# Kernel tuning notes

Hardware: AMD Instinct MI355X
Metric: run time of the kernel (lower is better)

The kernel has to match this reference:

```python
import jax, jax.numpy as jnp
import numpy as np

D_STATE = 16
D_CONV = 4
DT_RANK = 2  # ceil(d_model/16) with d_model=32


def _conv2d(x, w, b, pad, dil=1, groups=1):
    y = jax.lax.conv_general_dilated(
        x, w, (1, 1), ((pad, pad), (pad, pad)), rhs_dilation=(dil, dil),
        feature_group_count=groups, dimension_numbers=('NCHW', 'OIHW', 'NCHW'))
    return y + b[None, :, None, None]


def _ssm(xc, delta, A, Bc, Cc, D):
    # xc,delta: (B,L,Di); A: (Di,N); Bc,Cc: (B,L,N)
    dA = jnp.exp(delta[..., None] * A)                       # (B,L,Di,N)
    dBx = delta[..., None] * Bc[:, :, None, :] * xc[..., None]
    def comb(e1, e2):
        a1, b1 = e1
        a2, b2 = e2
        return a2 * a1, a2 * b1 + b2
    _, h = jax.lax.associative_scan(comb, (dA, dBx), axis=1)  # h_t = dA_t*h_{t-1}+dBx_t
    return jnp.einsum('bldn,bln->bld', h, Cc) + xc * D


def _dir(xin, cw, cb, wx, wdt, bdt, A_log, D):
    # causal depthwise conv1d over L, then silu
    L = xin.shape[1]
    xp = jnp.pad(xin, ((0, 0), (D_CONV - 1, 0), (0, 0)))
    xc = sum(xp[:, k:k + L, :] * cw[:, k] for k in range(D_CONV)) + cb
    xc = jax.nn.silu(xc)
    dbc = xc @ wx.T                                          # (B,L,dt_rank+2N)
    dt, Bc, Cc = jnp.split(dbc, [DT_RANK, DT_RANK + D_STATE], axis=-1)
    delta = jax.nn.softplus(dt @ wdt.T + bdt)
    return _ssm(xc, delta, -jnp.exp(A_log), Bc, Cc, D)


def _mamba(xn, w_in, cwf, cbf, wxf, wdtf, bdtf, Af, Df,
           cwb, cbb, wxb, wdtb, bdtb, Ab, Db, w_out):
    xz = xn @ w_in.T                                         # (B,L,2*Di)
    xin, z = jnp.split(xz, 2, axis=-1)
    y_f = _dir(xin, cwf, cbf, wxf, wdtf, bdtf, Af, Df)
    y_b = jnp.flip(_dir(jnp.flip(xin, axis=1), cwb, cbb, wxb, wdtb, bdtb, Ab, Db), axis=1)
    return ((y_f + y_b) * jax.nn.silu(z)) @ w_out.T          # bimamba v2: sum of directions


def _forward(x, w_att, b_att, ln_w, ln_b, w_in,
             conv_w_f, conv_b_f, wx_f, wdt_f, bdt_f, A_log_f, D_f,
             conv_w_b, conv_b_b, wx_b, wdt_b, bdt_b, A_log_b, D_b,
             w_out, w_se, b_se, w_conv, b_conv):
    B, C, H, W = x.shape
    att1 = x
    xa = _conv2d(x, w_att, b_att, pad=9, dil=3, groups=C)    # dilated depthwise, same HxW
    xf = xa.reshape(B, C, H * W).transpose(0, 2, 1)          # (B,L,C)
    mu = xf.mean(-1, keepdims=True)
    var = xf.var(-1, keepdims=True)
    xn = (xf - mu) / jnp.sqrt(var + 1e-5) * ln_w + ln_b
    out = _mamba(xn, w_in, conv_w_f, conv_b_f, wx_f, wdt_f, bdt_f, A_log_f, D_f,
                 conv_w_b, conv_b_b, wx_b, wdt_b, bdt_b, A_log_b, D_b, w_out)
    att2 = out.transpose(0, 2, 1).reshape(B, C, H, W)
    att = jnp.concatenate([att1, att2], axis=1)
    pooled = jnp.concatenate([att.mean(1, keepdims=True), att.max(1, keepdims=True)], axis=1)
    se = jax.nn.sigmoid(_conv2d(pooled, w_se, b_se, pad=3))
    output = att1 * se[:, 0:1] + att2 * se[:, 1:2]
    return _conv2d(output, w_conv, b_conv, pad=1)


def setup_inputs() -> dict:
    key = jax.random.key(0)
    ks = jax.random.split(key, 16)
    B, C, H, W = 4, 32, 96, 96
    Di, OUT = 64, 64
    n = jax.random.normal
    A_log = jnp.tile(jnp.log(jnp.arange(1, D_STATE + 1, dtype=jnp.float32)), (Di, 1))
    return {
        'x': n(ks[0], (B, C, H, W), jnp.float32),
        'w_att': n(ks[1], (C, 1, 7, 7), jnp.float32) * 0.05,
        'b_att': jnp.zeros((C,), jnp.float32),
        'ln_w': jnp.ones((C,), jnp.float32),
        'ln_b': jnp.zeros((C,), jnp.float32),
        'w_in': n(ks[2], (2 * Di, C), jnp.float32) / np.sqrt(C),
        'conv_w_f': n(ks[3], (Di, D_CONV), jnp.float32) * 0.3,
        'conv_b_f': jnp.zeros((Di,), jnp.float32),
        'wx_f': n(ks[4], (DT_RANK + 2 * D_STATE, Di), jnp.float32) / np.sqrt(Di),
        'wdt_f': n(ks[5], (Di, DT_RANK), jnp.float32) * 0.5,
        'bdt_f': n(ks[6], (Di,), jnp.float32) * 0.1,
        'A_log_f': A_log,
        'D_f': jnp.ones((Di,), jnp.float32),
        'conv_w_b': n(ks[7], (Di, D_CONV), jnp.float32) * 0.3,
        'conv_b_b': jnp.zeros((Di,), jnp.float32),
        'wx_b': n(ks[8], (DT_RANK + 2 * D_STATE, Di), jnp.float32) / np.sqrt(Di),
        'wdt_b': n(ks[9], (Di, DT_RANK), jnp.float32) * 0.5,
        'bdt_b': n(ks[10], (Di,), jnp.float32) * 0.1,
        'A_log_b': A_log,
        'D_b': jnp.ones((Di,), jnp.float32),
        'w_out': n(ks[11], (C, Di), jnp.float32) / np.sqrt(Di),
        'w_se': n(ks[12], (2, 2, 7, 7), jnp.float32) * 0.1,
        'b_se': jnp.zeros((2,), jnp.float32),
        'w_conv': n(ks[13], (OUT, C, 3, 3), jnp.float32) * 0.06,
        'b_conv': jnp.zeros((OUT,), jnp.float32),
    }


def reference(x, w_att, b_att, ln_w, ln_b, w_in,
              conv_w_f, conv_b_f, wx_f, wdt_f, bdt_f, A_log_f, D_f,
              conv_w_b, conv_b_b, wx_b, wdt_b, bdt_b, A_log_b, D_b,
              w_out, w_se, b_se, w_conv, b_conv):
    return _forward(x, w_att, b_att, ln_w, ln_b, w_in,
                    conv_w_f, conv_b_f, wx_f, wdt_f, bdt_f, A_log_f, D_f,
                    conv_w_b, conv_b_b, wx_b, wdt_b, bdt_b, A_log_b, D_b,
                    w_out, w_se, b_se, w_conv, b_conv)
```

## Files before the change

### kernel.cpp

```cpp
#include <hip/hip_runtime.h>
#include <math.h>

#define BB 4
#define CH 32
#define HH 96
#define WW 96
#define LL (HH*WW)
#define DI 64
#define NS 16
#define BL (BB*LL)
#define NCH 288
#define CLEN (LL/NCH)
#define GG 8

__device__ __forceinline__ float sigmoidf_(float x){ return 1.f/(1.f+__expf(-x)); }
__device__ __forceinline__ float siluf_(float x){ return x*sigmoidf_(x); }
__device__ __forceinline__ float softplusf_(float x){
  return (x > 15.f) ? x : __logf(1.f + __expf(x));
}
#define WAVE_LDS_FENCE() do { asm volatile("s_waitcnt lgkmcnt(0)" ::: "memory"); __builtin_amdgcn_sched_barrier(0); } while(0)

__global__ __launch_bounds__(256) void k1_conv_att(
    const float* __restrict__ x, const float* __restrict__ w,
    const float* __restrict__ bias, float* __restrict__ xa){
  int idx = blockIdx.x*256 + threadIdx.x;
  if (idx >= BB*CH*LL) return;
  int w0 = idx % WW; int h0 = (idx/WW) % HH; int c = (idx/LL) % CH;
  const float* xp = x + (idx/LL)*LL;
  const float* wp = w + c*49;
  float acc = bias[c];
  #pragma unroll
  for (int kh=0; kh<7; ++kh){
    int hh = h0 + 3*kh - 9;
    if ((unsigned)hh >= HH) continue;
    const float* row = xp + hh*WW;
    #pragma unroll
    for (int kw=0; kw<7; ++kw){
      int ww = w0 + 3*kw - 9;
      if ((unsigned)ww < WW) acc += row[ww]*wp[kh*7+kw];
    }
  }
  xa[idx] = acc;
}

__global__ __launch_bounds__(128) void k2_ln_inproj(
    const float* __restrict__ xa, const float* __restrict__ w_in,
    const float* __restrict__ ln_w, const float* __restrict__ ln_b,
    float* __restrict__ xin, float* __restrict__ zs){
  __shared__ float xs[CH*36];
  __shared__ float smu[32], srs[32];
  int tid = threadIdx.x;
  int tg0 = blockIdx.x*32;
  int bb = tg0 / LL;
  int l0 = tg0 % LL;
  const float* xab = xa + bb*CH*LL + l0;
  for (int r=0; r<8; ++r){
    int idx = r*128 + tid;
    int c = idx >> 5, t = idx & 31;
    xs[c*36+t] = xab[c*LL + t];
  }
  int j = tid;
  float wlj[CH];
  float swl=0.f, bj=0.f;
  #pragma unroll
  for (int c=0;c<CH;++c){
    float wv = ln_w[c]*w_in[j*CH+c];
    wlj[c] = wv; swl += wv;
    bj += ln_b[c]*w_in[j*CH+c];
  }
  __syncthreads();
  if (tid < 32){
    float s=0.f, s2=0.f;
    #pragma unroll
    for (int c=0;c<CH;++c){ float v = xs[c*36+tid]; s+=v; s2+=v*v; }
    float mu = s*(1.f/CH);
    float var = s2*(1.f/CH) - mu*mu;
    smu[tid]=mu; srs[tid]=rsqrtf(var+1e-5f);
  }
  __syncthreads();
  for (int t4=0;t4<8;++t4){
    float a0=0.f,a1=0.f,a2=0.f,a3=0.f;
    #pragma unroll
    for (int c=0;c<CH;++c){
      float4 xv = *(const float4*)&xs[c*36 + t4*4];
      float wv = wlj[c];
      a0 += xv.x*wv; a1 += xv.y*wv; a2 += xv.z*wv; a3 += xv.w*wv;
    }
    float av[4] = {a0,a1,a2,a3};
    #pragma unroll
    for (int q=0;q<4;++q){
      int t = t4*4+q;
      float out = srs[t]*(av[q] - smu[t]*swl) + bj;
      int base = ((bb*LL) + l0 + t)*DI;
      if (j < DI) xin[base + j] = out;
      else        zs[base + (j-DI)] = siluf_(out);
    }
  }
}

__global__ __launch_bounds__(64) void k3_fused(
    const float* __restrict__ xin,
    const float* __restrict__ cw_f, const float* __restrict__ cb_f,
    const float* __restrict__ wx_f, const float* __restrict__ wdt_f, const float* __restrict__ bdt_f,
    const float* __restrict__ Al_f, const float* __restrict__ D_f,
    const float* __restrict__ cw_b, const float* __restrict__ cb_b,
    const float* __restrict__ wx_b, const float* __restrict__ wdt_b, const float* __restrict__ bdt_b,
    const float* __restrict__ Al_b, const float* __restrict__ D_b,
    float* __restrict__ yl_f, float* __restrict__ sp_f, float* __restrict__ Cc_f,
    float* __restrict__ yl_b, float* __restrict__ sp_b, float* __restrict__ Cc_b,
    float* __restrict__ aggP, float* __restrict__ aggS){
  int lane = threadIdx.x;
  int dir = blockIdx.y;
  int bb = blockIdx.z;
  int ch = blockIdx.x;
  int p0 = ch*CLEN;
  const float* cw  = dir? cw_b : cw_f;
  const float* cb  = dir? cb_b : cb_f;
  const float* wx  = dir? wx_b : wx_f;
  const float* wdt = dir? wdt_b : wdt_f;
  const float* bdt = dir? bdt_b : bdt_f;
  const float* Al  = dir? Al_b : Al_f;
  const float* Dv  = dir? D_b : D_f;
  float* ylbuf = dir? yl_b : yl_f;
  float* spbuf = dir? sp_b : sp_f;
  float* Ccb   = dir? Cc_b : Cc_f;

  __shared__ float xcs[GG*64];
  __shared__ float bcs[GG*16];
  __shared__ float ccs[GG*16];
  __shared__ float dtb[GG*2];

  int d = lane;
  float c0=cw[d*4+0], c1=cw[d*4+1], c2=cw[d*4+2], c3=cw[d*4+3], cbv=cb[d];
  float wd0=wdt[d*2], wd1=wdt[d*2+1], bd=bdt[d];
  float Dd = Dv[d];
  float A[NS];
  #pragma unroll
  for (int n4=0;n4<4;++n4){
    float4 av = *(const float4*)&Al[d*NS + n4*4];
    A[n4*4+0] = -__expf(av.x); A[n4*4+1] = -__expf(av.y);
    A[n4*4+2] = -__expf(av.z); A[n4*4+3] = -__expf(av.w);
  }
  float wreg[64];
  if (lane < 34){
    #pragma unroll
    for (int c4=0;c4<16;++c4){
      float4 wv = *(const float4*)&wx[lane*64 + c4*4];
      wreg[c4*4+0]=wv.x; wreg[c4*4+1]=wv.y; wreg[c4*4+2]=wv.z; wreg[c4*4+3]=wv.w;
    }
  }
  float S[NS];
  #pragma unroll
  for (int n=0;n<NS;++n) S[n]=0.f;
  float sdl = 0.f;
  float u1=0.f,u2=0.f,u3=0.f;
  #pragma unroll
  for (int k=1;k<=3;++k){
    int pos = p0 - k;
    float v = 0.f;
    if (pos >= 0){ int ls = dir? (LL-1-pos) : pos; v = xin[(bb*LL+ls)*DI + d]; }
    if(k==1) u1=v; else if(k==2) u2=v; else u3=v;
  }

  const int NG = CLEN/GG;
  float u0buf[GG], u0nxt[GG];
  #pragma unroll
  for (int j=0;j<GG;++j){
    int pos = p0 + j;
    int ls = dir? (LL-1-pos) : pos;
    u0buf[j] = xin[(bb*LL+ls)*DI + d];
  }
  #pragma unroll
  for (int g=0; g<NG; ++g){
    int pbase = p0 + g*GG;
    if (g+1 < NG){
      #pragma unroll
      for (int j=0;j<GG;++j){
        int pos = pbase + GG + j;
        int ls = dir? (LL-1-pos) : pos;
        u0nxt[j] = xin[(bb*LL+ls)*DI + d];
      }
    }
    float xcr[GG];
    #pragma unroll
    for (int j=0;j<GG;++j){
      float u0 = u0buf[j];
      float xc = siluf_(cbv + c0*u3 + c1*u2 + c2*u1 + c3*u0);
      u3=u2; u2=u1; u1=u0;
      xcr[j] = xc;
      xcs[j*64+d] = xc;
    }
    WAVE_LDS_FENCE();
    if (lane < 34){
      #pragma unroll
      for (int j=0;j<GG;++j){
        float acc = 0.f;
        #pragma unroll
        for (int c4=0;c4<16;++c4){
          float4 xv = *(const float4*)&xcs[j*64 + c4*4];
          acc += xv.x*wreg[c4*4+0] + xv.y*wreg[c4*4+1]
               + xv.z*wreg[c4*4+2] + xv.w*wreg[c4*4+3];
        }
        int tb = bb*LL + pbase + j;
        if (lane < 2){
          dtb[j*2+lane] = acc;
        } else if (lane < 18){
          bcs[j*16 + lane-2] = acc;
        } else {
          Ccb[tb*NS + lane-18] = acc;
          ccs[j*16 + lane-18] = acc;
        }
      }
    }
    WAVE_LDS_FENCE();
    #pragma unroll
    for (int j=0;j<GG;++j){
      int tb = bb*LL + pbase + j;
      float dlt = softplusf_(dtb[j*2]*wd0 + dtb[j*2+1]*wd1 + bd);
      sdl += dlt;
      spbuf[tb*DI + d] = sdl;
      float dx = dlt*xcr[j];
      float yv = xcr[j]*Dd;
      #pragma unroll
      for (int n4=0;n4<4;++n4){
        float4 bv = *(const float4*)&bcs[j*16 + n4*4];
        float4 cv = *(const float4*)&ccs[j*16 + n4*4];
        float bvv[4] = {bv.x,bv.y,bv.z,bv.w};
        float cvv[4] = {cv.x,cv.y,cv.z,cv.w};
        #pragma unroll
        for (int q=0;q<4;++q){
          int n = n4*4+q;
          float dA = __expf(dlt*A[n]);
          S[n] = dA*S[n] + dx*bvv[q];
          yv += S[n]*cvv[q];
        }
      }
      ylbuf[tb*DI + d] = yv;
    }
    #pragma unroll
    for (int j=0;j<GG;++j) u0buf[j] = u0nxt[j];
  }
  int bdd = (bb*2+dir)*DI + d;
  float* pp = aggP + (bdd*NCH + ch)*NS;
  float* sp = aggS + (bdd*NCH + ch)*NS;
  #pragma unroll
  for (int n4=0;n4<4;++n4){
    *(float4*)&pp[n4*4] = make_float4(__expf(A[n4*4+0]*sdl),__expf(A[n4*4+1]*sdl),
                                      __expf(A[n4*4+2]*sdl),__expf(A[n4*4+3]*sdl));
    *(float4*)&sp[n4*4] = make_float4(S[n4*4+0],S[n4*4+1],S[n4*4+2],S[n4*4+3]);
  }
}

__global__ __launch_bounds__(256) void p2_scan_agg(
    const float* __restrict__ aggP, const float* __restrict__ aggS,
    float* __restrict__ hin){
  int t = blockIdx.x*256 + threadIdx.x;
  if (t >= BB*2*DI*NS) return;
  int bdd = t >> 4, n = t & 15;
  float h = 0.f;
  #pragma unroll 4
  for (int k=0;k<NCH;++k){
    int i = (bdd*NCH + k)*NS + n;
    float pv = aggP[i], sv = aggS[i];
    hin[i] = h;
    h = pv*h + sv;
  }
}

__global__ __launch_bounds__(256) void k4_outproj(
    const float* __restrict__ yl_f, const float* __restrict__ yl_b,
    const float* __restrict__ sp_f, const float* __restrict__ sp_b,
    const float* __restrict__ Cc_f, const float* __restrict__ Cc_b,
    const float* __restrict__ Al_f, const float* __restrict__ Al_b,
    const float* __restrict__ hin, const float* __restrict__ zs,
    const float* __restrict__ w_out, float* __restrict__ att2){
  __shared__ float ccs_f[32*16], ccs_b[32*16];
  __shared__ float gt[32*64];
  __shared__ float wol[32*65];
  __shared__ float ot[32*33];
  int tid = threadIdx.x;
  int tg0 = blockIdx.x*32;
  int bb = tg0/LL, l0 = tg0%LL;
  int d = tid & 63, tslot = tid >> 6;
  for (int r=0;r<8;++r){
    int idx = r*256+tid;
    wol[(idx>>6)*65 + (idx&63)] = w_out[idx];
  }
  {
    int base_f = (bb*LL + l0)*NS;
    int base_b = (bb*LL + (LL-32-l0))*NS;
    #pragma unroll
    for (int r=0;r<2;++r){
      int idx = r*256+tid;
      ccs_f[idx] = Cc_f[base_f+idx];
      ccs_b[idx] = Cc_b[base_b+idx];
    }
  }
  int ch_f = l0/CLEN;
  int ch_b = (LL-32-l0)/CLEN;
  const float* hpf = hin + (((bb*2+0)*DI + d)*NCH + ch_f)*NS;
  const float* hpb = hin + (((bb*2+1)*DI + d)*NCH + ch_b)*NS;
  float Af[NS], Ab[NS], hf[NS], hb[NS];
  #pragma unroll
  for (int n4=0;n4<4;++n4){
    float4 av = *(const float4*)&Al_f[d*NS + n4*4];
    Af[n4*4+0]=-__expf(av.x); Af[n4*4+1]=-__expf(av.y);
    Af[n4*4+2]=-__expf(av.z); Af[n4*4+3]=-__expf(av.w);
    float4 aw = *(const float4*)&Al_b[d*NS + n4*4];
    Ab[n4*4+0]=-__expf(aw.x); Ab[n4*4+1]=-__expf(aw.y);
    Ab[n4*4+2]=-__expf(aw.z); Ab[n4*4+3]=-__expf(aw.w);
    float4 hv = *(const float4*)&hpf[n4*4];
    hf[n4*4+0]=hv.x; hf[n4*4+1]=hv.y; hf[n4*4+2]=hv.z; hf[n4*4+3]=hv.w;
    float4 hw = *(const float4*)&hpb[n4*4];
    hb[n4*4+0]=hw.x; hb[n4*4+1]=hw.y; hb[n4*4+2]=hw.z; hb[n4*4+3]=hw.w;
  }
  __syncthreads();
  #pragma unroll
  for (int r=0;r<8;++r){
    int tk = tslot*8 + r;
    int l = l0 + tk;
    int tf  = (bb*LL + l)*DI + d;
    int tb2 = (bb*LL + (LL-1-l))*DI + d;
    float spf = sp_f[tf],  yf = yl_f[tf];
    float spb = sp_b[tb2], yb = yl_b[tb2];
    int jb = 31 - tk;
    float fixf = 0.f, fixb = 0.f;
    #pragma unroll
    for (int n=0;n<NS;++n){
      fixf += ccs_f[tk*16+n] * (hf[n]*__expf(Af[n]*spf));
      fixb += ccs_b[jb*16+n] * (hb[n]*__expf(Ab[n]*spb));
    }
    gt[tk*64+d] = (yf+fixf + yb+fixb) * zs[tf];
  }
  __syncthreads();
  int c = tid & 31, tsl = tid >> 5;
  for (int tg=0; tg<4; ++tg){
    int tk = tg*8+tsl;
    float acc=0.f;
    #pragma unroll
    for (int dd=0;dd<DI;++dd) acc += gt[tk*64+dd]*wol[c*65+dd];
    ot[c*33+tk] = acc;
  }
  __syncthreads();
  float* a2 = att2 + bb*CH*LL + l0;
  for (int r=0;r<4;++r){
    int idx = r*256+tid;
    int cc2 = idx>>5, t = idx&31;
    a2[cc2*LL + t] = ot[cc2*33+t];
  }
}

__global__ __launch_bounds__(256) void k5a_pool(
    const float* __restrict__ x, const float* __restrict__ att2, float* __restrict__ pooled){
  __shared__ float ps[4][64], pm[4][64];
  int tid = threadIdx.x;
  int lq = tid & 63, q = tid >> 6;
  int gl = blockIdx.x*64 + lq;
  int bb = gl/LL, l = gl%LL;
  const float* xp = x + bb*CH*LL + l;
  const float* ap = att2 + bb*CH*LL + l;
  float s=0.f, m=-INFINITY;
  #pragma unroll
  for (int cc=0;cc<8;++cc){
    int c = q*8+cc;
    float v1 = xp[c*LL], v2 = ap[c*LL];
    s += v1+v2;
    m = fmaxf(m, fmaxf(v1,v2));
  }
  ps[q][lq] = s; pm[q][lq] = m;
  __syncthreads();
  if (tid < 64){
    int gl2 = blockIdx.x*64 + tid;
    int bb2 = gl2/LL, l2 = gl2%LL;
    float ss = (ps[0][tid]+ps[1][tid]) + (ps[2][tid]+ps[3][tid]);
    float mm = fmaxf(fmaxf(pm[0][tid],pm[1][tid]), fmaxf(pm[2][tid],pm[3][tid]));
    pooled[(bb2*2+0)*LL + l2] = ss*(1.f/64.f);
    pooled[(bb2*2+1)*LL + l2] = mm;
  }
}

__global__ __launch_bounds__(256) void k5b_se_combine(
    const float* __restrict__ x, const float* __restrict__ att2,
    const float* __restrict__ pooled, const float* __restrict__ w_se,
    const float* __restrict__ b_se, float* __restrict__ outbuf){
  __shared__ float pb[4][64];
  __shared__ float sep[2][64];
  int tid = threadIdx.x;
  int lq = tid & 63, q = tid >> 6;
  int i = q & 1, o = q >> 1;
  int gl = blockIdx.x*64 + lq;
  int bb = gl/LL, l = gl%LL;
  int h0 = l/WW, w0 = l%WW;
  const float* pp = pooled + (bb*2+i)*LL;
  const float* wp = w_se + (o*2+i)*49;
  float a = 0.f;
  #pragma unroll
  for (int kh=0;kh<7;++kh){
    int hh = h0+kh-3; if((unsigned)hh>=HH) continue;
    const float* row = pp + hh*WW;
    #pragma unroll
    for (int kw=0;kw<7;++kw){
      int ww2 = w0+kw-3;
      if((unsigned)ww2<WW) a += row[ww2]*wp[kh*7+kw];
    }
  }
  pb[q][lq] = a;
  __syncthreads();
  if (tid < 128){
    int oo = tid >> 6, l2 = tid & 63;
    sep[oo][l2] = sigmoidf_(b_se[oo] + pb[oo*2+0][l2] + pb[oo*2+1][l2]);
  }
  __syncthreads();
  float se0 = sep[0][lq], se1 = sep[1][lq];
  const float* xp = x + bb*CH*LL + l;
  const float* ap = att2 + bb*CH*LL + l;
  float* op = outbuf + bb*CH*LL + l;
  #pragma unroll
  for (int cc=0;cc<8;++cc){
    int c = q*8+cc;
    op[c*LL] = xp[c*LL]*se0 + ap[c*LL]*se1;
  }
}

__global__ __launch_bounds__(256) void k6_conv3x3(
    const float* __restrict__ inb, const float* __restrict__ wc,
    const float* __restrict__ bc, float* __restrict__ out){
  __shared__ float lds[CH*3*98];
  int tid = threadIdx.x;
  int h = blockIdx.x, cohalf = blockIdx.y, bb = blockIdx.z;
  const float* ib = inb + bb*CH*LL;
  for (int r=0; r<36; ++r){
    int idx = r*256+tid;
    int ci = idx/(3*96); int rr = (idx/96)%3; int ww2 = idx%96;
    int hh = h + rr - 1;
    float v = ((unsigned)hh < HH) ? ib[ci*LL + hh*WW + ww2] : 0.f;
    lds[(ci*3+rr)*98 + 1 + ww2] = v;
  }
  if (tid < 96){
    int ci = tid/3, rr = tid%3;
    lds[(ci*3+rr)*98 + 0]  = 0.f;
    lds[(ci*3+rr)*98 + 97] = 0.f;
  }
  __syncthreads();
  int coslot = tid >> 4, wslot = tid & 15;
  int co0 = cohalf*32 + coslot*2, wb = wslot*6;
  float acc[2][6];
  #pragma unroll
  for (int q=0;q<2;++q)
    #pragma unroll
    for (int j2=0;j2<6;++j2) acc[q][j2]=0.f;
  for (int ci=0; ci<CH; ++ci){
    float wt[2][9];
    #pragma unroll
    for (int q=0;q<2;++q){
      const float* wp = wc + ((co0+q)*CH + ci)*9;
      #pragma unroll
      for (int k=0;k<9;++k) wt[q][k] = wp[k];
    }
    #pragma unroll
    for (int kh=0;kh<3;++kh){
      const float* row = &lds[(ci*3+kh)*98 + wb];
      float s[8];
      #pragma unroll
      for (int t2=0;t2<8;++t2) s[t2] = row[t2];
      #pragma unroll
      for (int q=0;q<2;++q)
        #pragma unroll
        for (int kw=0;kw<3;++kw){
          float wv = wt[q][kh*3+kw];
          #pragma unroll
          for (int j2=0;j2<6;++j2) acc[q][j2] += s[j2+kw]*wv;
        }
    }
  }
  #pragma unroll
  for (int q=0;q<2;++q){
    int co = co0+q;
    float bv = bc[co];
    float* op = out + (bb*64 + co)*LL + h*WW + wb;
    #pragma unroll
    for (int j2=0;j2<6;++j2) op[j2] = acc[q][j2]+bv;
  }
}

extern "C" void kernel_launch(void* const* d_in, const int* in_sizes, int n_in,
                              void* d_out, int out_size, void* d_ws, size_t ws_size,
                              hipStream_t stream){
  const float* x     = (const float*)d_in[0];
  const float* w_att = (const float*)d_in[1];
  const float* b_att = (const float*)d_in[2];
  const float* ln_w  = (const float*)d_in[3];
  const float* ln_b  = (const float*)d_in[4];
  const float* w_in  = (const float*)d_in[5];
  const float* cw_f  = (const float*)d_in[6];
  const float* cb_f  = (const float*)d_in[7];
  const float* wx_f  = (const float*)d_in[8];
  const float* wdt_f = (const float*)d_in[9];
  const float* bdt_f = (const float*)d_in[10];
  const float* Al_f  = (const float*)d_in[11];
  const float* D_f   = (const float*)d_in[12];
  const float* cw_b  = (const float*)d_in[13];
  const float* cb_b  = (const float*)d_in[14];
  const float* wx_b  = (const float*)d_in[15];
  const float* wdt_b = (const float*)d_in[16];
  const float* bdt_b = (const float*)d_in[17];
  const float* Al_b  = (const float*)d_in[18];
  const float* D_b   = (const float*)d_in[19];
  const float* w_out = (const float*)d_in[20];
  const float* w_se  = (const float*)d_in[21];
  const float* b_se  = (const float*)d_in[22];
  const float* w_conv= (const float*)d_in[23];
  const float* b_conv= (const float*)d_in[24];

  float* ws = (float*)d_ws;
  float* xa     = ws + 0;
  float* att2   = ws + 0;
  float* xin    = ws + 1179648;
  float* outbuf = ws + 1179648;
  float* zs     = ws + 3538944;
  float* yl_f   = ws + 5898240;
  float* yl_b   = ws + 8257536;
  float* sp_f   = ws + 10616832;
  float* sp_b   = ws + 12976128;
  float* Cc_f   = ws + 15335424;
  float* Cc_b   = ws + 15925248;
  float* aggP   = ws + 16515072;
  float* aggS   = ws + 18874368;
  float* hin    = ws + 21233664;
  float* pooled = ws + 23592960;

  k1_conv_att<<<4608,256,0,stream>>>(x, w_att, b_att, xa);
  k2_ln_inproj<<<1152,128,0,stream>>>(xa, w_in, ln_w, ln_b, xin, zs);
  k3_fused<<<dim3(NCH,2,BB),64,0,stream>>>(xin,
      cw_f,cb_f,wx_f,wdt_f,bdt_f,Al_f,D_f,
      cw_b,cb_b,wx_b,wdt_b,bdt_b,Al_b,D_b,
      yl_f,sp_f,Cc_f, yl_b,sp_b,Cc_b, aggP,aggS);
  p2_scan_agg<<<32,256,0,stream>>>(aggP,aggS,hin);
  k4_outproj<<<1152,256,0,stream>>>(yl_f,yl_b, sp_f,sp_b, Cc_f,Cc_b,
      Al_f,Al_b, hin, zs, w_out, att2);
  k5a_pool<<<576,256,0,stream>>>(x, att2, pooled);
  k5b_se_combine<<<576,256,0,stream>>>(x, att2, pooled, w_se, b_se, outbuf);
  k6_conv3x3<<<dim3(HH,2,BB),256,0,stream>>>(outbuf, w_conv, b_conv, (float*)d_out);
}
```

Baseline: 342.9 us.

## Double scan chunk count and split x-projection across full wavefront with shuffles

Doubles the number of SSM scan chunks per sequence so CLEN halves to 16, and shrinks the per-group batch to 4 positions. The x_proj matvec is now spread over all 64 lanes: each lane computes half of a B/C row, combined with a cross-half shuffle. The two dt rows are computed with a full-wave shuffle reduction in place of a shared-memory round trip. The chunk scan writes hin in place over aggP, and k4_outproj adjusts chunk indexing because 32-position tiles now span two chunks. The intent is more parallelism and less serial work per wavefront in the fused scan kernel. The cost is a longer serial aggregate scan, the per-position shuffle reductions, and dropping the prefetch of inputs.

```diff
diff --git a/kernel.cpp b/kernel.cpp
--- a/kernel.cpp
+++ b/kernel.cpp
@@ -9,9 +9,9 @@
 #define DI 64
 #define NS 16
 #define BL (BB*LL)
-#define NCH 288
+#define NCH 576
 #define CLEN (LL/NCH)
-#define GG 8
+#define GG 4
 
 __device__ __forceinline__ float sigmoidf_(float x){ return 1.f/(1.f+__expf(-x)); }
 __device__ __forceinline__ float siluf_(float x){ return x*sigmoidf_(x); }
@@ -128,7 +128,6 @@
   __shared__ float xcs[GG*64];
   __shared__ float bcs[GG*16];
   __shared__ float ccs[GG*16];
-  __shared__ float dtb[GG*2];
 
   int d = lane;
   float c0=cw[d*4+0], c1=cw[d*4+1], c2=cw[d*4+2], c3=cw[d*4+3], cbv=cb[d];
@@ -141,14 +140,15 @@
     A[n4*4+0] = -__expf(av.x); A[n4*4+1] = -__expf(av.y);
     A[n4*4+2] = -__expf(av.z); A[n4*4+3] = -__expf(av.w);
   }
-  float wreg[64];
-  if (lane < 34){
-    #pragma unroll
-    for (int c4=0;c4<16;++c4){
-      float4 wv = *(const float4*)&wx[lane*64 + c4*4];
-      wreg[c4*4+0]=wv.x; wreg[c4*4+1]=wv.y; wreg[c4*4+2]=wv.z; wreg[c4*4+3]=wv.w;
-    }
-  }
+  int prow = 2 + (lane & 31);
+  int chalf = lane >> 5;
+  float wreg[32];
+  #pragma unroll
+  for (int i4=0;i4<8;++i4){
+    float4 wv = *(const float4*)&wx[prow*64 + chalf*32 + i4*4];
+    wreg[i4*4+0]=wv.x; wreg[i4*4+1]=wv.y; wreg[i4*4+2]=wv.z; wreg[i4*4+3]=wv.w;
+  }
+  float wx0l = wx[d], wx1l = wx[64+d];
   float S[NS];
   #pragma unroll
   for (int n=0;n<NS;++n) S[n]=0.f;
@@ -163,52 +163,44 @@
   }
 
   const int NG = CLEN/GG;
-  float u0buf[GG], u0nxt[GG];
-  #pragma unroll
-  for (int j=0;j<GG;++j){
-    int pos = p0 + j;
-    int ls = dir? (LL-1-pos) : pos;
-    u0buf[j] = xin[(bb*LL+ls)*DI + d];
-  }
-  #pragma unroll
   for (int g=0; g<NG; ++g){
     int pbase = p0 + g*GG;
-    if (g+1 < NG){
-      #pragma unroll
-      for (int j=0;j<GG;++j){
-        int pos = pbase + GG + j;
-        int ls = dir? (LL-1-pos) : pos;
-        u0nxt[j] = xin[(bb*LL+ls)*DI + d];
-      }
-    }
-    float xcr[GG];
+    float xcr[GG], dlt[GG];
     #pragma unroll
     for (int j=0;j<GG;++j){
-      float u0 = u0buf[j];
+      int pos = pbase + j;
+      int ls = dir? (LL-1-pos) : pos;
+      float u0 = xin[(bb*LL+ls)*DI + d];
       float xc = siluf_(cbv + c0*u3 + c1*u2 + c2*u1 + c3*u0);
       u3=u2; u2=u1; u1=u0;
       xcr[j] = xc;
       xcs[j*64+d] = xc;
+      float pp0 = xc*wx0l, pp1 = xc*wx1l;
+      #pragma unroll
+      for (int i=1;i<64;i<<=1){
+        pp0 += __shfl_xor(pp0, i, 64);
+        pp1 += __shfl_xor(pp1, i, 64);
+      }
+      dlt[j] = softplusf_(pp0*wd0 + pp1*wd1 + bd);
     }
     WAVE_LDS_FENCE();
-    if (lane < 34){
+    #pragma unroll
+    for (int j=0;j<GG;++j){
+      float acc = 0.f;
       #pragma unroll
-      for (int j=0;j<GG;++j){
-        float acc = 0.f;
-        #pragma unroll
-        for (int c4=0;c4<16;++c4){
-          float4 xv = *(const float4*)&xcs[j*64 + c4*4];
-          acc += xv.x*wreg[c4*4+0] + xv.y*wreg[c4*4+1]
-               + xv.z*wreg[c4*4+2] + xv.w*wreg[c4*4+3];
-        }
-        int tb = bb*LL + pbase + j;
-        if (lane < 2){
-          dtb[j*2+lane] = acc;
-        } else if (lane < 18){
-          bcs[j*16 + lane-2] = acc;
+      for (int c4=0;c4<8;++c4){
+        float4 xv = *(const float4*)&xcs[j*64 + chalf*32 + c4*4];
+        acc += xv.x*wreg[c4*4+0] + xv.y*wreg[c4*4+1]
+             + xv.z*wreg[c4*4+2] + xv.w*wreg[c4*4+3];
+      }
+      float full = acc + __shfl_xor(acc, 32, 64);
+      if (lane < 32){
+        if (lane < 16){
+          bcs[j*16 + lane] = full;
         } else {
-          Ccb[tb*NS + lane-18] = acc;
-          ccs[j*16 + lane-18] = acc;
+          int n = lane - 16;
+          ccs[j*16 + n] = full;
+          Ccb[(bb*LL + pbase + j)*NS + n] = full;
         }
       }
     }
@@ -216,10 +208,10 @@
     #pragma unroll
     for (int j=0;j<GG;++j){
       int tb = bb*LL + pbase + j;
-      float dlt = softplusf_(dtb[j*2]*wd0 + dtb[j*2+1]*wd1 + bd);
-      sdl += dlt;
+      float dl = dlt[j];
+      sdl += dl;
       spbuf[tb*DI + d] = sdl;
-      float dx = dlt*xcr[j];
+      float dx = dl*xcr[j];
       float yv = xcr[j]*Dd;
       #pragma unroll
       for (int n4=0;n4<4;++n4){
@@ -230,15 +222,13 @@
         #pragma unroll
         for (int q=0;q<4;++q){
           int n = n4*4+q;
-          float dA = __expf(dlt*A[n]);
+          float dA = __expf(dl*A[n]);
           S[n] = dA*S[n] + dx*bvv[q];
           yv += S[n]*cvv[q];
         }
       }
       ylbuf[tb*DI + d] = yv;
     }
-    #pragma unroll
-    for (int j=0;j<GG;++j) u0buf[j] = u0nxt[j];
   }
   int bdd = (bb*2+dir)*DI + d;
   float* pp = aggP + (bdd*NCH + ch)*NS;
@@ -252,8 +242,7 @@
 }
 
 __global__ __launch_bounds__(256) void p2_scan_agg(
-    const float* __restrict__ aggP, const float* __restrict__ aggS,
-    float* __restrict__ hin){
+    const float* aggP, const float* aggS, float* hin){
   int t = blockIdx.x*256 + threadIdx.x;
   if (t >= BB*2*DI*NS) return;
   int bdd = t >> 4, n = t & 15;
@@ -296,8 +285,8 @@
       ccs_b[idx] = Cc_b[base_b+idx];
     }
   }
-  int ch_f = l0/CLEN;
-  int ch_b = (LL-32-l0)/CLEN;
+  int ch_f = l0/CLEN + (tslot>>1);
+  int ch_b = (LL-l0)/CLEN - 1 - (tslot>>1);
   const float* hpf = hin + (((bb*2+0)*DI + d)*NCH + ch_f)*NS;
   const float* hpb = hin + (((bb*2+1)*DI + d)*NCH + ch_b)*NS;
   float Af[NS], Ab[NS], hf[NS], hb[NS];
@@ -525,9 +514,9 @@
   float* Cc_f   = ws + 15335424;
   float* Cc_b   = ws + 15925248;
   float* aggP   = ws + 16515072;
-  float* aggS   = ws + 18874368;
-  float* hin    = ws + 21233664;
-  float* pooled = ws + 23592960;
+  float* aggS   = ws + 21233664;
+  float* hin    = aggP;
+  float* pooled = ws + 25952256;
 
   k1_conv_att<<<4608,256,0,stream>>>(x, w_att, b_att, xa);
   k2_ln_inproj<<<1152,128,0,stream>>>(xa, w_in, ln_w, ln_b, xin, zs);
```

Result: slower. 375.1 us (+9.4%).
